# Performance work log

Measured on AMD Instinct MI355X. Metric: run time of the kernel, lower is better.

Reference implementation:

```python
import jax, jax.numpy as jnp
import numpy as np


def setup_inputs() -> dict:
    key = jax.random.key(0)
    ks = jax.random.split(key, 8)
    B, S, H = 4, 2048, 1024
    heads = 16
    lim = 1.0 / np.sqrt(H)  # nn.Linear default init range
    x = jax.random.normal(ks[0], (B, S, H), dtype=jnp.float32)
    atten_mask = jnp.zeros((B, 1, S, 1), dtype=jnp.float32)  # 1.0 marks padded positions
    Wq = jax.random.uniform(ks[1], (H, H), jnp.float32, -lim, lim)
    bq = jax.random.uniform(ks[2], (H,), jnp.float32, -lim, lim)
    Wk = jax.random.uniform(ks[3], (H, H), jnp.float32, -lim, lim)
    bk = jax.random.uniform(ks[4], (H,), jnp.float32, -lim, lim)
    Wv = jax.random.uniform(ks[5], (H, H), jnp.float32, -lim, lim)
    bv = jax.random.uniform(ks[6], (H,), jnp.float32, -lim, lim)
    return {"x": x, "Wq": Wq, "bq": bq, "Wk": Wk, "bk": bk, "Wv": Wv, "bv": bv,
            "atten_mask": atten_mask, "attention_head_num": 16}


def reference(x, Wq, bq, Wk, bk, Wv, bv, atten_mask, attention_head_num):
    B, S, H = x.shape
    h = attention_head_num
    d = H // h
    # QKV projections (torch Linear: x @ W.T + b)
    q = (x @ Wq.T + bq).reshape(B, S, h, d).transpose(0, 2, 1, 3)  # [B,h,S,d]
    k = (x @ Wk.T + bk).reshape(B, S, h, d).transpose(0, 2, 1, 3)
    v = (x @ Wv.T + bv).reshape(B, S, h, d).transpose(0, 2, 1, 3)
    # combined padding + look-ahead mask: True -> masked
    causal = jnp.triu(jnp.ones((S, S), dtype=atten_mask.dtype), 1)  # [S,S]
    mask = (atten_mask + causal) >= 1.0  # [B,1 or h,S,S] broadcast
    mask = jnp.broadcast_to(mask, (B, h, S, S))
    scale = 1.0 / jnp.sqrt(jnp.asarray(d, dtype=jnp.float32))
    scores = jnp.einsum('bhqd,bhkd->bhqk', q, k) * scale
    scores = jnp.where(mask, jnp.float32(-1e9), scores)
    att = jax.nn.softmax(scores, axis=-1)
    out = jnp.einsum('bhqk,bhkd->bhqd', att, v)  # [B,h,S,d]
    return out.transpose(0, 2, 1, 3).reshape(B, S, H)
```

## Files before the change

### kernel.cpp

```cpp
#include <hip/hip_runtime.h>
#include <hip/hip_bf16.h>
#include <stdint.h>

typedef short v8s __attribute__((ext_vector_type(8)));
typedef float v4f __attribute__((ext_vector_type(4)));
typedef unsigned long long u64;
typedef unsigned short u16;
typedef unsigned int u32;
typedef u64 v2u __attribute__((ext_vector_type(2)));

__device__ __forceinline__ u16 f2bf(float f) {
    unsigned u = __builtin_bit_cast(unsigned, f);
    u += 0x7FFFu + ((u >> 16) & 1u);
    return (u16)(u >> 16);
}

__device__ __forceinline__ u32 cvt_pk_bf16(float lo, float hi) {
    u32 r;
    asm("v_cvt_pk_bf16_f32 %0, %1, %2" : "=v"(r) : "v"(lo), "v"(hi));
    return r;
}

__device__ __forceinline__ float ex2(float x) {
    float r;
    asm("v_exp_f32 %0, %1" : "=v"(r) : "v"(x));
    return r;
}

__device__ __forceinline__ void gload_lds16(const void* g, const void* lds) {
    __builtin_amdgcn_global_load_lds(
        (const __attribute__((address_space(1))) unsigned int*)(unsigned long long)g,
        (__attribute__((address_space(3))) unsigned int*)(unsigned int)(unsigned long long)lds,
        16, 0, 0);
}

__global__ __launch_bounds__(256) void cvt_all(const float* __restrict__ x,
                                               const float* __restrict__ wq,
                                               const float* __restrict__ wk,
                                               const float* __restrict__ wv,
                                               u16* __restrict__ xb, u16* __restrict__ wqb,
                                               u16* __restrict__ wkb, u16* __restrict__ wvb) {
    int i = blockIdx.x * 256 + threadIdx.x;
    const float* in;
    u16* out;
    if (i < 2097152)      { in = x;  out = xb; }
    else if (i < 2359296) { in = wq; out = wqb; i -= 2097152; }
    else if (i < 2621440) { in = wk; out = wkb; i -= 2359296; }
    else                  { in = wv; out = wvb; i -= 2621440; }
    float4 v = ((const float4*)in)[i];
    ((ushort4*)out)[i] = make_ushort4(f2bf(v.x), f2bf(v.y), f2bf(v.z), f2bf(v.w));
}

__global__ __launch_bounds__(256, 4)
void qkv_gemm_all(const u16* __restrict__ X,
                  const u16* __restrict__ Wq, const u16* __restrict__ Wk, const u16* __restrict__ Wv,
                  const float* __restrict__ bq, const float* __restrict__ bk, const float* __restrict__ bv,
                  u16* __restrict__ Qg, u16* __restrict__ Kg, u16* __restrict__ VTg) {
    __shared__ __align__(16) char smem[34816];
    char* ldsA = smem;
    char* ldsB = smem + 16384;
    u16*  ldsE = (u16*)smem;

    const int l = (blockIdx.x & 7) * 192 + (blockIdx.x >> 3);
    const int mode = l >> 9;
    const int bx = l & 511;
    const u16* W = (mode == 0) ? Wq : (mode == 1) ? Wk : Wv;
    const float* bias = (mode == 0) ? bq : (mode == 1) ? bk : bv;
    u16* Out = (mode == 0) ? Qg : (mode == 1) ? Kg : VTg;

    const int t = threadIdx.x;
    const int lane = t & 63, wave = t >> 6;
    const int lhi = lane >> 4, llo = lane & 15;
    const int wm = wave >> 1, wn = wave & 1;
    const int m0 = (bx >> 3) * 128;
    const int n0 = (bx & 7) * 128;

    const int srow = (t * 16) >> 7;
    const int ssc = ((t * 16) >> 4) & 7;
    v4f acc[4][4] = {};

    for (int k0 = 0; k0 < 1024; k0 += 64) {
        #pragma unroll
        for (int i = 0; i < 4; ++i) {
            int row = i * 32 + srow;
            int c = ssc ^ (row & 7);
            const char* wbaseA = ldsA + (i * 256 + wave * 64) * 16;
            const char* wbaseB = ldsB + (i * 256 + wave * 64) * 16;
            gload_lds16(X + (m0 + row) * 1024 + k0 + c * 8, wbaseA);
            gload_lds16(W + (n0 + row) * 1024 + k0 + c * 8, wbaseB);
        }
        __syncthreads();
        __builtin_amdgcn_s_setprio(1);
        #pragma unroll
        for (int s = 0; s < 2; ++s) {
            v8s af[4], bf[4];
            #pragma unroll
            for (int i = 0; i < 4; ++i) {
                int r = wm * 64 + i * 16 + llo;
                af[i] = *(const v8s*)(ldsA + r * 128 + (((lhi + 4 * s) ^ (r & 7)) << 4));
            }
            #pragma unroll
            for (int j = 0; j < 4; ++j) {
                int r = wn * 64 + j * 16 + llo;
                bf[j] = *(const v8s*)(ldsB + r * 128 + (((lhi + 4 * s) ^ (r & 7)) << 4));
            }
            #pragma unroll
            for (int i = 0; i < 4; ++i)
                #pragma unroll
                for (int j = 0; j < 4; ++j)
                    acc[i][j] = __builtin_amdgcn_mfma_f32_16x16x32_bf16(af[i], bf[j], acc[i][j], 0, 0, 0);
        }
        __builtin_amdgcn_s_setprio(0);
        __syncthreads();
    }

    float bv_[4];
    #pragma unroll
    for (int j = 0; j < 4; ++j) bv_[j] = bias[n0 + wn * 64 + j * 16 + llo];
    const float scl = (mode == 0) ? 0.18033688011112042f : 1.0f;

    #pragma unroll
    for (int i = 0; i < 4; ++i) {
        #pragma unroll
        for (int j = 0; j < 4; ++j) {
            #pragma unroll
            for (int r = 0; r < 4; ++r) {
                int ml = wm * 64 + i * 16 + lhi * 4 + r;
                int nl = wn * 64 + j * 16 + llo;
                float v = (acc[i][j][r] + bv_[j]) * scl;
                u16 hh = f2bf(v);
                if (mode == 2) ldsE[nl * 136 + ml] = hh;
                else           ldsE[ml * 136 + nl] = hh;
            }
        }
    }
    __syncthreads();

    const int row = t >> 1, half = t & 1;
    if (mode == 2) {
        int n = n0 + row, hh = n >> 6, dd = n & 63;
        int b = m0 >> 11, sbase = (m0 & 2047) + half * 64;
        u16* dst = Out + ((b * 16 + hh) * 64 + dd) * 2048 + sbase;
        #pragma unroll
        for (int j = 0; j < 8; ++j)
            *(v8s*)(dst + j * 8) = *(const v8s*)&ldsE[row * 136 + half * 64 + j * 8];
    } else {
        int m = m0 + row, b = m >> 11, s = m & 2047;
        int hh = (n0 + half * 64) >> 6;
        u16* dst = Out + ((b * 16 + hh) * 2048 + s) * 64;
        #pragma unroll
        for (int j = 0; j < 8; ++j)
            *(v8s*)(dst + j * 8) = *(const v8s*)&ldsE[row * 136 + half * 64 + j * 8];
    }
}

__global__ __launch_bounds__(256, 4)
void flash_attn(const u16* __restrict__ Qg, const u16* __restrict__ Kg,
                const u16* __restrict__ VTg, const float* __restrict__ am,
                float* __restrict__ out) {
    __shared__ __align__(16) char smem[40960];
    char* ldsK = smem;
    char* ldsV = smem + 16384;
    char* ldsP = smem + 32768 + (threadIdx.x >> 6) * 2048;

    const int t = threadIdx.x;
    const int lane = t & 63, wave = t >> 6;
    const int lhi = lane >> 4, llo = lane & 15;
    const int bh = blockIdx.x;
    const int qi = 31 - blockIdx.y;
    const int b = bh >> 4, h = bh & 15;
    const int qw = qi * 64 + wave * 16;
    const int q = qw + llo;

    v8s qf[2];
    #pragma unroll
    for (int s = 0; s < 2; ++s)
        qf[s] = *(const v8s*)(Qg + (bh * 2048 + q) * 64 + lhi * 8 + 32 * s);

    v8s ones;
    #pragma unroll
    for (int j = 0; j < 8; ++j) ones[j] = (short)0x3F80;

    const float rowpen = am[b * 2048 + q];

    const int pswz = (llo & 7) << 4;

    const int srow = (t * 16) >> 7, ssc = ((t * 16) >> 4) & 7;
    const int sc1 = ssc ^ (srow & 7), sc2 = ssc ^ ((srow + 32) & 7);
    #define STAGE(buf, kj2) do {                                                   \
        const int kv0_ = (kj2) * 64;                                               \
        const char* wbK = ldsK + (buf) * 8192 + (wave * 64) * 16;                  \
        const char* wbV = ldsV + (buf) * 8192 + (wave * 64) * 16;                  \
        gload_lds16(Kg + (bh * 2048 + kv0_ + srow) * 64 + sc1 * 8, wbK);           \
        gload_lds16(VTg + (bh * 64 + srow) * 2048 + kv0_ + sc1 * 8, wbV);          \
        gload_lds16(Kg + (bh * 2048 + kv0_ + srow + 32) * 64 + sc2 * 8, wbK + 4096); \
        gload_lds16(VTg + (bh * 64 + srow + 32) * 2048 + kv0_ + sc2 * 8, wbV + 4096); \
    } while (0)

    float mrow = -1e30f;
    v4f lsum_acc = {};
    v4f o_acc[4] = {};

    STAGE(0, 0);
    __syncthreads();

    for (int kj = 0; kj <= qi; ++kj) {
        const int cur = kj & 1;
        if (kj < qi) STAGE(cur ^ 1, kj + 1);
        const char* K = ldsK + cur * 8192;
        const char* V = ldsV + cur * 8192;
        const int kv0 = kj * 64;

        const int nt4 = (kj == qi) ? (wave + 1) : 4;
        v4f sacc[4] = {};
        __builtin_amdgcn_s_setprio(1);
        #pragma unroll
        for (int tt = 0; tt < 4; ++tt) {
            if (tt < nt4) {
                #pragma unroll
                for (int s = 0; s < 2; ++s) {
                    int row = tt * 16 + llo;
                    int c = lhi + 4 * s;
                    v8s kb = *(const v8s*)(K + row * 128 + ((c ^ (row & 7)) << 4));
                    sacc[tt] = __builtin_amdgcn_mfma_f32_16x16x32_bf16(kb, qf[s], sacc[tt], 0, 0, 0);
                }
            }
        }
        __builtin_amdgcn_s_setprio(0);

        if (kj == qi) {
            #pragma unroll
            for (int tt = 0; tt < 4; ++tt)
                #pragma unroll
                for (int r = 0; r < 4; ++r) {
                    int kvg = kv0 + tt * 16 + lhi * 4 + r;
                    if (kvg > q) sacc[tt][r] = -1e30f;
                }
        }
        if (rowpen >= 1.0f) {
            #pragma unroll
            for (int tt = 0; tt < 4; ++tt)
                #pragma unroll
                for (int r = 0; r < 4; ++r) sacc[tt][r] = -1e30f;
        }

        float m0_ = fmaxf(fmaxf(sacc[0][0], sacc[0][1]), sacc[0][2]);
        float m1_ = fmaxf(fmaxf(sacc[0][3], sacc[1][0]), sacc[1][1]);
        float m2_ = fmaxf(fmaxf(sacc[1][2], sacc[1][3]), sacc[2][0]);
        float m3_ = fmaxf(fmaxf(sacc[2][1], sacc[2][2]), sacc[2][3]);
        float m4_ = fmaxf(fmaxf(sacc[3][0], sacc[3][1]), fmaxf(sacc[3][2], sacc[3][3]));
        float lmx = fmaxf(fmaxf(fmaxf(m0_, m1_), fmaxf(m2_, m3_)), m4_);

        if (__any(lmx > mrow + 8.0f)) {
            float mx = fmaxf(lmx, __shfl_xor(lmx, 16));
            mx = fmaxf(mx, __shfl_xor(mx, 32));
            const float mn = fmaxf(mrow, mx);
            const float sc_o = ex2(mrow - mn);
            mrow = mn;
            #pragma unroll
            for (int r = 0; r < 4; ++r) lsum_acc[r] *= sc_o;
            #pragma unroll
            for (int dt = 0; dt < 4; ++dt)
                #pragma unroll
                for (int r = 0; r < 4; ++r) o_acc[dt][r] *= sc_o;
        }

        #pragma unroll
        for (int tt = 0; tt < 4; ++tt) {
            float p0 = ex2(sacc[tt][0] - mrow);
            float p1 = ex2(sacc[tt][1] - mrow);
            float p2 = ex2(sacc[tt][2] - mrow);
            float p3 = ex2(sacc[tt][3] - mrow);
            u32 w0 = cvt_pk_bf16(p0, p1);
            u32 w1 = cvt_pk_bf16(p2, p3);
            *(u64*)(ldsP + llo * 128 + ((tt * 32 + lhi * 8) ^ pswz)) = (u64)w0 | ((u64)w1 << 32);
        }

        __builtin_amdgcn_s_setprio(1);
        #pragma unroll
        for (int s = 0; s < 2; ++s) {
            const char* prow = ldsP + llo * 128 + ((lhi * 16 + s * 64) ^ pswz);
            u64 plo = *(const u64*)(prow);
            u64 phi = *(const u64*)(prow + 8);
            v2u tmp; tmp.x = plo; tmp.y = phi;
            v8s pb = __builtin_bit_cast(v8s, tmp);
            lsum_acc = __builtin_amdgcn_mfma_f32_16x16x32_bf16(ones, pb, lsum_acc, 0, 0, 0);
            #pragma unroll
            for (int dt = 0; dt < 4; ++dt) {
                int vrow = dt * 16 + llo;
                v8s vb = *(const v8s*)(V + vrow * 128 + (((lhi + 4 * s) ^ (vrow & 7)) << 4));
                o_acc[dt] = __builtin_amdgcn_mfma_f32_16x16x32_bf16(vb, pb, o_acc[dt], 0, 0, 0);
            }
        }
        __builtin_amdgcn_s_setprio(0);
        __syncthreads();
    }

    const float inv = 1.0f / lsum_acc[0];
    float* dst = out + (size_t)(b * 2048 + q) * 1024 + h * 64 + lhi * 4;
    #pragma unroll
    for (int dt = 0; dt < 4; ++dt) {
        float4 o;
        o.x = o_acc[dt][0] * inv;
        o.y = o_acc[dt][1] * inv;
        o.z = o_acc[dt][2] * inv;
        o.w = o_acc[dt][3] * inv;
        *(float4*)(dst + dt * 16) = o;
    }
}

extern "C" void kernel_launch(void* const* d_in, const int* in_sizes, int n_in,
                              void* d_out, int out_size, void* d_ws, size_t ws_size,
                              hipStream_t stream) {
    const float* x  = (const float*)d_in[0];
    const float* Wq = (const float*)d_in[1];
    const float* bq = (const float*)d_in[2];
    const float* Wk = (const float*)d_in[3];
    const float* bk = (const float*)d_in[4];
    const float* Wv = (const float*)d_in[5];
    const float* bv = (const float*)d_in[6];
    const float* amask = (const float*)d_in[7];
    float* out = (float*)d_out;

    char* ws = (char*)d_ws;
    u16* xb  = (u16*)(ws);
    u16* Wqb = (u16*)(ws + 16777216);
    u16* Wkb = (u16*)(ws + 16777216 + 2097152);
    u16* Wvb = (u16*)(ws + 16777216 + 2 * 2097152);
    u16* Qg  = (u16*)(ws + 23068672);
    u16* Kg  = (u16*)(ws + 39845888);
    u16* VTg = (u16*)(ws + 56623104);

    cvt_all<<<11264, 256, 0, stream>>>(x, Wq, Wk, Wv, xb, Wqb, Wkb, Wvb);
    qkv_gemm_all<<<1536, 256, 0, stream>>>(xb, Wqb, Wkb, Wvb, bq, bk, bv, Qg, Kg, VTg);
    flash_attn<<<dim3(64, 32), 256, 0, stream>>>(Qg, Kg, VTg, amask, out);
}
```

Baseline: 150.2 us.

## Software-pipeline QK^T of the next tile against softmax and PV of the current tile

Restructures the flash-attention loop so the QK^T MFMAs for tile i+1 are issued before the softmax and PV work for tile i. Two score register sets are alternated, and V gets a triple-buffered LDS ring while K stays double-buffered, with prefetch two tiles ahead. The aim is to overlap matrix-core work with exp/max VALU work and to hide global-load latency. In exchange, LDS grows to 48KB, register use rises, and launch bounds drop occupancy from 4 to 3 blocks per CU.

```diff
diff --git a/kernel.cpp b/kernel.cpp
--- a/kernel.cpp
+++ b/kernel.cpp
@@ -154,14 +154,14 @@
     }
 }
 
-__global__ __launch_bounds__(256, 4)
+__global__ __launch_bounds__(256, 3)
 void flash_attn(const u16* __restrict__ Qg, const u16* __restrict__ Kg,
                 const u16* __restrict__ VTg, const float* __restrict__ am,
                 float* __restrict__ out) {
-    __shared__ __align__(16) char smem[40960];
+    __shared__ __align__(16) char smem[49152];
     char* ldsK = smem;
     char* ldsV = smem + 16384;
-    char* ldsP = smem + 32768 + (threadIdx.x >> 6) * 2048;
+    char* ldsP = smem + 40960 + (threadIdx.x >> 6) * 2048;
 
     const int t = threadIdx.x;
     const int lane = t & 63, wave = t >> 6;
@@ -182,73 +182,70 @@
     for (int j = 0; j < 8; ++j) ones[j] = (short)0x3F80;
 
     const float rowpen = am[b * 2048 + q];
-
     const int pswz = (llo & 7) << 4;
 
     const int srow = (t * 16) >> 7, ssc = ((t * 16) >> 4) & 7;
     const int sc1 = ssc ^ (srow & 7), sc2 = ssc ^ ((srow + 32) & 7);
-    #define STAGE(buf, kj2) do {                                                   \
-        const int kv0_ = (kj2) * 64;                                               \
-        const char* wbK = ldsK + (buf) * 8192 + (wave * 64) * 16;                  \
-        const char* wbV = ldsV + (buf) * 8192 + (wave * 64) * 16;                  \
-        gload_lds16(Kg + (bh * 2048 + kv0_ + srow) * 64 + sc1 * 8, wbK);           \
-        gload_lds16(VTg + (bh * 64 + srow) * 2048 + kv0_ + sc1 * 8, wbV);          \
-        gload_lds16(Kg + (bh * 2048 + kv0_ + srow + 32) * 64 + sc2 * 8, wbK + 4096); \
-        gload_lds16(VTg + (bh * 64 + srow + 32) * 2048 + kv0_ + sc2 * 8, wbV + 4096); \
-    } while (0)
 
     float mrow = -1e30f;
     v4f lsum_acc = {};
     v4f o_acc[4] = {};
-
-    STAGE(0, 0);
-    __syncthreads();
-
-    for (int kj = 0; kj <= qi; ++kj) {
-        const int cur = kj & 1;
-        if (kj < qi) STAGE(cur ^ 1, kj + 1);
-        const char* K = ldsK + cur * 8192;
-        const char* V = ldsV + cur * 8192;
-        const int kv0 = kj * 64;
-
-        const int nt4 = (kj == qi) ? (wave + 1) : 4;
-        v4f sacc[4] = {};
+    v4f sacA[4], sacB[4];
+
+    auto stage = [&](int j) {
+        const int kv0_ = j * 64;
+        const char* wbK = ldsK + (j & 1) * 8192 + (wave * 64) * 16;
+        const char* wbV = ldsV + (j % 3) * 8192 + (wave * 64) * 16;
+        gload_lds16(Kg + (bh * 2048 + kv0_ + srow) * 64 + sc1 * 8, wbK);
+        gload_lds16(VTg + (bh * 64 + srow) * 2048 + kv0_ + sc1 * 8, wbV);
+        gload_lds16(Kg + (bh * 2048 + kv0_ + srow + 32) * 64 + sc2 * 8, wbK + 4096);
+        gload_lds16(VTg + (bh * 64 + srow + 32) * 2048 + kv0_ + sc2 * 8, wbV + 4096);
+    };
+
+    auto qkt = [&](v4f (&SN)[4], int tile) {
+        const char* K = ldsK + (tile & 1) * 8192;
+        const int ntq = (tile == qi) ? (wave + 1) : 4;
+        #pragma unroll
+        for (int tt = 0; tt < 4; ++tt) SN[tt] = (v4f){};
         __builtin_amdgcn_s_setprio(1);
         #pragma unroll
         for (int tt = 0; tt < 4; ++tt) {
-            if (tt < nt4) {
+            if (tt < ntq) {
                 #pragma unroll
                 for (int s = 0; s < 2; ++s) {
                     int row = tt * 16 + llo;
                     int c = lhi + 4 * s;
                     v8s kb = *(const v8s*)(K + row * 128 + ((c ^ (row & 7)) << 4));
-                    sacc[tt] = __builtin_amdgcn_mfma_f32_16x16x32_bf16(kb, qf[s], sacc[tt], 0, 0, 0);
+                    SN[tt] = __builtin_amdgcn_mfma_f32_16x16x32_bf16(kb, qf[s], SN[tt], 0, 0, 0);
                 }
             }
         }
         __builtin_amdgcn_s_setprio(0);
-
-        if (kj == qi) {
+    };
+
+    auto smpv = [&](v4f (&SC)[4], int tile) {
+        const int kv0 = tile * 64;
+        if (tile == qi) {
             #pragma unroll
             for (int tt = 0; tt < 4; ++tt)
                 #pragma unroll
                 for (int r = 0; r < 4; ++r) {
                     int kvg = kv0 + tt * 16 + lhi * 4 + r;
-                    if (kvg > q) sacc[tt][r] = -1e30f;
+                    if (kvg > q) SC[tt][r] = -1e30f;
                 }
         }
         if (rowpen >= 1.0f) {
             #pragma unroll
             for (int tt = 0; tt < 4; ++tt)
                 #pragma unroll
-                for (int r = 0; r < 4; ++r) sacc[tt][r] = -1e30f;
-        }
-
-        float m0_ = fmaxf(fmaxf(sacc[0][0], sacc[0][1]), sacc[0][2]);
-        float m1_ = fmaxf(fmaxf(sacc[0][3], sacc[1][0]), sacc[1][1]);
-        float m2_ = fmaxf(fmaxf(sacc[1][2], sacc[1][3]), sacc[2][0]);
-        float m3_ = fmaxf(fmaxf(sacc[2][1], sacc[2][2]), sacc[2][3]);
-        float m4_ = fmaxf(fmaxf(sacc[3][0], sacc[3][1]), fmaxf(sacc[3][2], sacc[3][3]));
+                for (int r = 0; r < 4; ++r) SC[tt][r] = -1e30f;
+        }
+
+        float m0_ = fmaxf(fmaxf(SC[0][0], SC[0][1]), SC[0][2]);
+        float m1_ = fmaxf(fmaxf(SC[0][3], SC[1][0]), SC[1][1]);
+        float m2_ = fmaxf(fmaxf(SC[1][2], SC[1][3]), SC[2][0]);
+        float m3_ = fmaxf(fmaxf(SC[2][1], SC[2][2]), SC[2][3]);
+        float m4_ = fmaxf(fmaxf(SC[3][0], SC[3][1]), fmaxf(SC[3][2], SC[3][3]));
         float lmx = fmaxf(fmaxf(fmaxf(m0_, m1_), fmaxf(m2_, m3_)), m4_);
 
         if (__any(lmx > mrow + 8.0f)) {
@@ -267,15 +264,16 @@
 
         #pragma unroll
         for (int tt = 0; tt < 4; ++tt) {
-            float p0 = ex2(sacc[tt][0] - mrow);
-            float p1 = ex2(sacc[tt][1] - mrow);
-            float p2 = ex2(sacc[tt][2] - mrow);
-            float p3 = ex2(sacc[tt][3] - mrow);
+            float p0 = ex2(SC[tt][0] - mrow);
+            float p1 = ex2(SC[tt][1] - mrow);
+            float p2 = ex2(SC[tt][2] - mrow);
+            float p3 = ex2(SC[tt][3] - mrow);
             u32 w0 = cvt_pk_bf16(p0, p1);
             u32 w1 = cvt_pk_bf16(p2, p3);
             *(u64*)(ldsP + llo * 128 + ((tt * 32 + lhi * 8) ^ pswz)) = (u64)w0 | ((u64)w1 << 32);
         }
 
+        const char* V = ldsV + (tile % 3) * 8192;
         __builtin_amdgcn_s_setprio(1);
         #pragma unroll
         for (int s = 0; s < 2; ++s) {
@@ -293,7 +291,26 @@
             }
         }
         __builtin_amdgcn_s_setprio(0);
+    };
+
+    stage(0);
+    stage(1);
+    __syncthreads();
+    qkt(sacA, 0);
+    __syncthreads();
+
+    int i = 0;
+    for (;;) {
+        if (i + 1 <= qi) qkt(sacB, i + 1);
+        if (i + 2 <= qi) stage(i + 2);
+        smpv(sacA, i);
         __syncthreads();
+        if (++i > qi) break;
+        if (i + 1 <= qi) qkt(sacA, i + 1);
+        if (i + 2 <= qi) stage(i + 2);
+        smpv(sacB, i);
+        __syncthreads();
+        if (++i > qi) break;
     }
 
     const float inv = 1.0f / lsum_acc[0];
```

Result: slower. 160.6 us (+6.9%).
